# Kernel tuning notes

Measured on AMD Instinct MI355X. Metric: run time of the kernel, lower is better.

Reference implementation:

```python
import jax, jax.numpy as jnp
import numpy as np

N, E, F, H, C, G = 100000, 1600000, 128, 64, 40, 2048


def setup_inputs() -> dict:
    key = jax.random.key(0)
    ks = jax.random.split(key, 8)
    x = jax.random.normal(ks[0], (N, F), dtype=jnp.float32)
    edge_index = jax.random.randint(ks[1], (2, E), 0, N, dtype=jnp.int64)
    batch = jnp.sort(jax.random.randint(ks[2], (N,), 0, G, dtype=jnp.int64))
    def glorot(k, shp):
        fan_in, fan_out = shp
        s = jnp.sqrt(2.0 / (fan_in + fan_out))
        return jax.random.normal(k, shp, dtype=jnp.float32) * s
    return {
        "x": x, "edge_index": edge_index, "batch": batch,
        "pre_w": glorot(ks[3], (F, H)), "pre_b": jnp.zeros((H,), jnp.float32),
        "c1_w": glorot(ks[4], (H, H)), "c1_b": jnp.zeros((H,), jnp.float32),
        "n1_g": jnp.ones((H,), jnp.float32), "n1_b": jnp.zeros((H,), jnp.float32),
        "c2_w": glorot(ks[5], (H, H)), "c2_b": jnp.zeros((H,), jnp.float32),
        "n2_g": jnp.ones((H,), jnp.float32), "n2_b": jnp.zeros((H,), jnp.float32),
        "post_w": glorot(ks[6], (H, C)), "post_b": jnp.zeros((C,), jnp.float32),
    }


def _gcn_conv(h, src, dst, deg_isqrt, W, b):
    # GCNConv with self-loops and symmetric D^{-1/2}(A+I)D^{-1/2} normalization.
    hw = h @ W                                        # [N, H]
    coef = deg_isqrt[src] * deg_isqrt[dst]            # [E]
    msg = hw[src] * coef[:, None]                     # gather + scale
    agg = jax.ops.segment_sum(msg, dst, num_segments=N)
    agg = agg + hw * (deg_isqrt * deg_isqrt)[:, None]  # self-loop term
    return agg + b


def _layer_norm(h, g, b, eps=1e-5):
    mu = jnp.mean(h, axis=-1, keepdims=True)
    var = jnp.mean(jnp.square(h - mu), axis=-1, keepdims=True)
    return (h - mu) * jax.lax.rsqrt(var + eps) * g + b


def reference(x, edge_index, batch, pre_w, pre_b, c1_w, c1_b, n1_g, n1_b,
              c2_w, c2_b, n2_g, n2_b, post_w, post_b):
    src, dst = edge_index[0], edge_index[1]
    ones = jnp.ones((E,), dtype=x.dtype)
    deg = jax.ops.segment_sum(ones, dst, num_segments=N) + 1.0  # +1 self-loop
    deg_isqrt = jax.lax.rsqrt(deg)

    h = x @ pre_w + pre_b                              # pre-process MLP
    h1 = jax.nn.relu(_layer_norm(_gcn_conv(h, src, dst, deg_isqrt, c1_w, c1_b), n1_g, n1_b))
    h2 = jax.nn.relu(_layer_norm(_gcn_conv(h1, src, dst, deg_isqrt, c2_w, c2_b), n2_g, n2_b))
    skip = h1 + h2                                     # sum of skip connections
    readout = jax.ops.segment_sum(skip, batch, num_segments=G)  # sum pooling
    return readout @ post_w + post_b                   # [G, C]
```

## Files before the change

### kernel.cpp

```cpp
#include <hip/hip_runtime.h>
#include <hip/hip_fp16.h>

#define NN 100000
#define NE 1600000
#define FIN 128
#define HD 64
#define CO 40
#define NG 2048
#define NSB 196
#define SCAP 9216
#define GCAP 13312
#define CHUNK 4096
#define NSCAT ((NE + CHUNK - 1) / CHUNK)

__global__ __launch_bounds__(256) void setup_kernel(int* __restrict__ scur,
                                                    float* __restrict__ readout,
                                                    unsigned int* __restrict__ dummy) {
    int gid = blockIdx.x * 256 + threadIdx.x;
    if (gid < NG * HD) readout[gid] = 0.0f;
    if (gid < NSB) scur[gid * 16] = gid * SCAP;
    if (gid < HD / 2) dummy[gid] = 0u;
}

__global__ __launch_bounds__(1024) void scatter_super(const int* __restrict__ src,
                                                      const int* __restrict__ dst,
                                                      int* __restrict__ scur,
                                                      unsigned int* __restrict__ stmp) {
    __shared__ int hist[NSB];
    __shared__ int gbase[NSB];
    int tid = threadIdx.x;
    int e0 = blockIdx.x * CHUNK;
    int d[4], s[4];
    if (tid < NSB) hist[tid] = 0;
    __syncthreads();
#pragma unroll
    for (int r = 0; r < 4; r++) {
        int e = e0 + tid + r * 1024;
        d[r] = -1; s[r] = 0;
        if (e < NE) {
            d[r] = dst[e];
            s[r] = src[e];
            atomicAdd(&hist[d[r] >> 9], 1);
        }
    }
    __syncthreads();
    if (tid < NSB) {
        int c = hist[tid];
        gbase[tid] = (c > 0) ? atomicAdd(&scur[tid * 16], c) : 0;
        hist[tid] = 0;
    }
    __syncthreads();
#pragma unroll
    for (int r = 0; r < 4; r++) {
        if (d[r] >= 0) {
            int b = d[r] >> 9;
            int p = atomicAdd(&hist[b], 1);
            stmp[gbase[b] + p] = ((unsigned int)(d[r] & 511) << 17) | (unsigned int)s[r];
        }
    }
}

__global__ __launch_bounds__(1024) void group_sort(const int* __restrict__ scur,
                                                   const unsigned int* __restrict__ stmp,
                                                   unsigned int* __restrict__ ssrc,
                                                   int* __restrict__ offs,
                                                   int* __restrict__ degn,
                                                   float* __restrict__ di) {
    __shared__ int lh[512];
    __shared__ int sc[512];
    __shared__ int lcur[512];
    int g = blockIdx.x;
    int tid = threadIdx.x;
    int base = g * SCAP;
    int cnt = scur[g * 16] - base;
    if (tid < 512) lh[tid] = 0;
    __syncthreads();
    unsigned int uv[9];
#pragma unroll
    for (int r = 0; r < 9; r++) {
        int i = tid + r * 1024;
        uv[r] = 0xFFFFFFFFu;
        if (i < cnt) {
            uv[r] = stmp[base + i];
            atomicAdd(&lh[uv[r] >> 17], 1);
        }
    }
    __syncthreads();
    int h = 0, pd = 0;
    if (tid < 512) {
        h = lh[tid];
        pd = (h + 7) & ~7;
        sc[tid] = pd;
    }
    __syncthreads();
    for (int off = 1; off < 512; off <<= 1) {
        int v = 0;
        if (tid >= off && tid < 512) v = sc[tid - off];
        __syncthreads();
        if (tid < 512) sc[tid] += v;
        __syncthreads();
    }
    if (tid < 512) {
        int excl = sc[tid] - pd;
        lcur[tid] = excl;
        int node = g * 512 + tid;
        if (node < NN) {
            offs[node] = g * GCAP + excl;
            degn[node] = pd;
            di[node] = rsqrtf((float)h + 1.0f);
        }
        size_t gb = (size_t)g * GCAP;
        for (int q = h; q < pd; q++) ssrc[gb + excl + q] = (unsigned int)NN;
    }
    __syncthreads();
#pragma unroll
    for (int r = 0; r < 9; r++) {
        unsigned int u = uv[r];
        if (u != 0xFFFFFFFFu) {
            int dl = (int)(u >> 17);
            int pos = atomicAdd(&lcur[dl], 1);
            ssrc[(size_t)g * GCAP + pos] = u & 0x1FFFFu;
        }
    }
}

__global__ __launch_bounds__(256) void weff_kernel(const float* __restrict__ pre_w,
                                                   const float* __restrict__ pre_b,
                                                   const float* __restrict__ c1_w,
                                                   float* __restrict__ weff,
                                                   float* __restrict__ beff) {
    if (blockIdx.x < 32) {
        int o = blockIdx.x * 256 + threadIdx.x;
        int r = o >> 6, c = o & 63;
        float acc = 0.0f;
#pragma unroll 8
        for (int k = 0; k < HD; k++) acc = fmaf(pre_w[r * HD + k], c1_w[k * HD + c], acc);
        weff[o] = acc;
    } else {
        int c = threadIdx.x;
        if (c < HD) {
            float acc = 0.0f;
#pragma unroll 8
            for (int k = 0; k < HD; k++) acc = fmaf(pre_b[k], c1_w[k * HD + c], acc);
            beff[c] = acc;
        }
    }
}

__global__ __launch_bounds__(256) void gemm1_tiled(const float* __restrict__ x,
                                                   const float* __restrict__ w,
                                                   const float* __restrict__ b,
                                                   const float* __restrict__ di,
                                                   __half* __restrict__ hws) {
    __shared__ float wS[FIN * HD];
    __shared__ float xS[64 * 64];
    int tid = threadIdx.x;
    for (int i = tid; i < FIN * HD; i += 256) wS[i] = w[i];
    int tn = tid & 15, tf = tid >> 4;
    int f0 = tf * 4;
    float4 bv = ((const float4*)b)[tf];
    int ntiles = (NN + 63) >> 6;
    for (int t = blockIdx.x; t < ntiles; t += gridDim.x) {
        int nb = t << 6;
        float acc[4][4];
#pragma unroll
        for (int i = 0; i < 4; i++)
#pragma unroll
            for (int j = 0; j < 4; j++) acc[i][j] = 0.0f;
        for (int kh = 0; kh < 2; kh++) {
            __syncthreads();
            {
                int n_l = tid >> 4;
                int k4l = tid & 15;
                for (int r = 0; r < 4; r++) {
                    int n = n_l + r * 16;
                    int row = nb + n;
                    float4 v = make_float4(0.f, 0.f, 0.f, 0.f);
                    if (row < NN) v = ((const float4*)(x + (size_t)row * FIN))[kh * 16 + k4l];
                    int g = n >> 2, nl2 = n & 3;
                    const float* vp = (const float*)&v;
#pragma unroll
                    for (int j = 0; j < 4; j++) {
                        int k = k4l * 4 + j;
                        int gp = g ^ (k & 15);
                        xS[k * 64 + gp * 4 + nl2] = vp[j];
                    }
                }
            }
            __syncthreads();
#pragma unroll 4
            for (int kl = 0; kl < 64; kl++) {
                int gp = tn ^ (kl & 15);
                float4 xv = *(const float4*)&xS[kl * 64 + gp * 4];
                float4 wv = *(const float4*)&wS[(kh * 64 + kl) * 64 + f0];
                acc[0][0] = fmaf(xv.x, wv.x, acc[0][0]); acc[0][1] = fmaf(xv.x, wv.y, acc[0][1]);
                acc[0][2] = fmaf(xv.x, wv.z, acc[0][2]); acc[0][3] = fmaf(xv.x, wv.w, acc[0][3]);
                acc[1][0] = fmaf(xv.y, wv.x, acc[1][0]); acc[1][1] = fmaf(xv.y, wv.y, acc[1][1]);
                acc[1][2] = fmaf(xv.y, wv.z, acc[1][2]); acc[1][3] = fmaf(xv.y, wv.w, acc[1][3]);
                acc[2][0] = fmaf(xv.z, wv.x, acc[2][0]); acc[2][1] = fmaf(xv.z, wv.y, acc[2][1]);
                acc[2][2] = fmaf(xv.z, wv.z, acc[2][2]); acc[2][3] = fmaf(xv.z, wv.w, acc[2][3]);
                acc[3][0] = fmaf(xv.w, wv.x, acc[3][0]); acc[3][1] = fmaf(xv.w, wv.y, acc[3][1]);
                acc[3][2] = fmaf(xv.w, wv.z, acc[3][2]); acc[3][3] = fmaf(xv.w, wv.w, acc[3][3]);
            }
        }
        int n0 = nb + tn * 4;
#pragma unroll
        for (int i = 0; i < 4; i++) {
            int n = n0 + i;
            if (n < NN) {
                float dn = di[n];
                __half2 p0 = __floats2half2_rn((acc[i][0] + bv.x) * dn, (acc[i][1] + bv.y) * dn);
                __half2 p1 = __floats2half2_rn((acc[i][2] + bv.z) * dn, (acc[i][3] + bv.w) * dn);
                __half2* o = (__half2*)(hws + (size_t)n * HD + f0);
                o[0] = p0; o[1] = p1;
            }
        }
    }
}

__global__ __launch_bounds__(256) void conv_gemm_tiled(const __half* __restrict__ hin,
                                                       const float* __restrict__ w,
                                                       const float* __restrict__ di,
                                                       __half* __restrict__ hws) {
    __shared__ float wS[HD * HD];
    __shared__ float xS[64 * HD];
    int tid = threadIdx.x;
    for (int i = tid; i < HD * HD; i += 256) wS[i] = w[i];
    int tn = tid & 15, tf = tid >> 4;
    int f0 = tf * 4;
    int ntiles = (NN + 63) >> 6;
    for (int t = blockIdx.x; t < ntiles; t += gridDim.x) {
        int nb = t << 6;
        __syncthreads();
        {
            int n_l = tid >> 3;
            int k8 = tid & 7;
            union U { float4 f4; __half2 h2[4]; } u;
            for (int r = 0; r < 2; r++) {
                int n = n_l + r * 32;
                int row = nb + n;
                u.f4 = make_float4(0.f, 0.f, 0.f, 0.f);
                if (row < NN) u.f4 = ((const float4*)(hin + (size_t)row * HD))[k8];
                int g = n >> 2, nl2 = n & 3;
#pragma unroll
                for (int j = 0; j < 4; j++) {
                    float2 p = __half22float2(u.h2[j]);
                    int k = k8 * 8 + 2 * j;
                    int gp = g ^ (k & 15);
                    xS[k * 64 + gp * 4 + nl2] = p.x;
                    int k2 = k + 1;
                    int gp2 = g ^ (k2 & 15);
                    xS[k2 * 64 + gp2 * 4 + nl2] = p.y;
                }
            }
        }
        __syncthreads();
        float acc[4][4];
#pragma unroll
        for (int i = 0; i < 4; i++)
#pragma unroll
            for (int j = 0; j < 4; j++) acc[i][j] = 0.0f;
#pragma unroll 4
        for (int k = 0; k < HD; k++) {
            int gp = tn ^ (k & 15);
            float4 xv = *(const float4*)&xS[k * 64 + gp * 4];
            float4 wv = *(const float4*)&wS[k * 64 + f0];
            acc[0][0] = fmaf(xv.x, wv.x, acc[0][0]); acc[0][1] = fmaf(xv.x, wv.y, acc[0][1]);
            acc[0][2] = fmaf(xv.x, wv.z, acc[0][2]); acc[0][3] = fmaf(xv.x, wv.w, acc[0][3]);
            acc[1][0] = fmaf(xv.y, wv.x, acc[1][0]); acc[1][1] = fmaf(xv.y, wv.y, acc[1][1]);
            acc[1][2] = fmaf(xv.y, wv.z, acc[1][2]); acc[1][3] = fmaf(xv.y, wv.w, acc[1][3]);
            acc[2][0] = fmaf(xv.z, wv.x, acc[2][0]); acc[2][1] = fmaf(xv.z, wv.y, acc[2][1]);
            acc[2][2] = fmaf(xv.z, wv.z, acc[2][2]); acc[2][3] = fmaf(xv.z, wv.w, acc[2][3]);
            acc[3][0] = fmaf(xv.w, wv.x, acc[3][0]); acc[3][1] = fmaf(xv.w, wv.y, acc[3][1]);
            acc[3][2] = fmaf(xv.w, wv.z, acc[3][2]); acc[3][3] = fmaf(xv.w, wv.w, acc[3][3]);
        }
        int n0 = nb + tn * 4;
#pragma unroll
        for (int i = 0; i < 4; i++) {
            int n = n0 + i;
            if (n < NN) {
                float dn = di[n];
                __half2 p0 = __floats2half2_rn(acc[i][0] * dn, acc[i][1] * dn);
                __half2 p1 = __floats2half2_rn(acc[i][2] * dn, acc[i][3] * dn);
                __half2* o = (__half2*)(hws + (size_t)n * HD + f0);
                o[0] = p0; o[1] = p1;
            }
        }
    }
}

__device__ __forceinline__ void gather_node8(const int* __restrict__ offs,
                                             const int* __restrict__ pdeg,
                                             const unsigned int* __restrict__ ssrc,
                                             const __half* __restrict__ hws,
                                             int node, int fp, float acc[8]) {
    int i0 = offs[node];
    int deg = pdeg[node];
    const uint4* ip = (const uint4*)(ssrc + i0);
    union U { float4 f4; __half2 h2[4]; } u[8];
    __half2 hacc[4][4];
#pragma unroll
    for (int s = 0; s < 4; s++)
#pragma unroll
        for (int t = 0; t < 4; t++) hacc[s][t] = __floats2half2_rn(0.f, 0.f);
    u[0].f4 = ((const float4*)(hws + (size_t)node * HD))[fp];
#pragma unroll
    for (int t = 0; t < 4; t++) hacc[0][t] = u[0].h2[t];
    int nit = deg >> 3;
    if (nit > 0) {
        uint4 a0 = ip[0], b0 = ip[1];
        uint4 a1 = make_uint4(0u, 0u, 0u, 0u), b1 = a1;
        if (nit > 1) { a1 = ip[2]; b1 = ip[3]; }
        for (int it = 0; it < nit; ++it) {
            bool more = (it + 2 < nit);
            uint4 a2 = a1, b2 = b1;
            if (more) { a2 = ip[2 * it + 4]; b2 = ip[2 * it + 5]; }
            u[0].f4 = ((const float4*)(hws + (size_t)a0.x * HD))[fp];
            u[1].f4 = ((const float4*)(hws + (size_t)a0.y * HD))[fp];
            u[2].f4 = ((const float4*)(hws + (size_t)a0.z * HD))[fp];
            u[3].f4 = ((const float4*)(hws + (size_t)a0.w * HD))[fp];
            u[4].f4 = ((const float4*)(hws + (size_t)b0.x * HD))[fp];
            u[5].f4 = ((const float4*)(hws + (size_t)b0.y * HD))[fp];
            u[6].f4 = ((const float4*)(hws + (size_t)b0.z * HD))[fp];
            u[7].f4 = ((const float4*)(hws + (size_t)b0.w * HD))[fp];
#pragma unroll
            for (int q = 0; q < 8; q++)
#pragma unroll
                for (int t = 0; t < 4; t++)
                    hacc[q & 3][t] = __hadd2(hacc[q & 3][t], u[q].h2[t]);
            a0 = a1; b0 = b1;
            a1 = a2; b1 = b2;
        }
    }
#pragma unroll
    for (int t = 0; t < 4; t++) {
        float2 a = __half22float2(hacc[0][t]);
        float2 b = __half22float2(hacc[1][t]);
        float2 c = __half22float2(hacc[2][t]);
        float2 d = __half22float2(hacc[3][t]);
        acc[2 * t]     = (a.x + b.x) + (c.x + d.x);
        acc[2 * t + 1] = (a.y + b.y) + (c.y + d.y);
    }
}

__device__ __forceinline__ void ln8(float v[8], int fp,
                                    const float* __restrict__ g,
                                    const float* __restrict__ bb,
                                    float y[8]) {
    float su = 0.0f;
#pragma unroll
    for (int t = 0; t < 8; t++) su += v[t];
    su += __shfl_xor(su, 1, 64); su += __shfl_xor(su, 2, 64); su += __shfl_xor(su, 4, 64);
    float mu = su * (1.0f / HD);
    float q = 0.0f;
#pragma unroll
    for (int t = 0; t < 8; t++) { float d = v[t] - mu; q += d * d; }
    q += __shfl_xor(q, 1, 64); q += __shfl_xor(q, 2, 64); q += __shfl_xor(q, 4, 64);
    float rstd = rsqrtf(q * (1.0f / HD) + 1e-5f);
    float4 ga = ((const float4*)g)[fp * 2], gb = ((const float4*)g)[fp * 2 + 1];
    float4 ba = ((const float4*)bb)[fp * 2], bc = ((const float4*)bb)[fp * 2 + 1];
    float gv[8] = {ga.x, ga.y, ga.z, ga.w, gb.x, gb.y, gb.z, gb.w};
    float bv[8] = {ba.x, ba.y, ba.z, ba.w, bc.x, bc.y, bc.z, bc.w};
#pragma unroll
    for (int t = 0; t < 8; t++) y[t] = fmaxf((v[t] - mu) * rstd * gv[t] + bv[t], 0.0f);
}

__global__ __launch_bounds__(256, 4) void gather_ln(const int* __restrict__ offs,
                                                    const int* __restrict__ pdeg,
                                                    const unsigned int* __restrict__ ssrc,
                                                    const float* __restrict__ di,
                                                    const __half* __restrict__ hws,
                                                    const float* __restrict__ cb,
                                                    const float* __restrict__ g,
                                                    const float* __restrict__ bb,
                                                    __half* __restrict__ out) {
    int wv = threadIdx.x >> 6;
    int lane = threadIdx.x & 63;
    int fp = lane & 7, gg = lane >> 3;
    int node = blockIdx.x * 32 + wv * 8 + gg;
    float acc[8];
    gather_node8(offs, pdeg, ssrc, hws, node, fp, acc);
    float4 ca = ((const float4*)cb)[fp * 2], cc = ((const float4*)cb)[fp * 2 + 1];
    float cv[8] = {ca.x, ca.y, ca.z, ca.w, cc.x, cc.y, cc.z, cc.w};
    float dn = di[node];
    float v[8], y[8];
#pragma unroll
    for (int t = 0; t < 8; t++) v[t] = acc[t] * dn + cv[t];
    ln8(v, fp, g, bb, y);
    union U { float4 f4; __half2 h2[4]; } u;
#pragma unroll
    for (int t = 0; t < 4; t++) u.h2[t] = __floats2half2_rn(y[2 * t], y[2 * t + 1]);
    ((float4*)(out + (size_t)node * HD))[fp] = u.f4;
}

__global__ __launch_bounds__(256, 4) void gather_ln_pool(const int* __restrict__ offs,
                                                         const int* __restrict__ pdeg,
                                                         const unsigned int* __restrict__ ssrc,
                                                         const float* __restrict__ di,
                                                         const __half* __restrict__ hws,
                                                         const float* __restrict__ cb,
                                                         const float* __restrict__ g,
                                                         const float* __restrict__ bb,
                                                         const __half* __restrict__ h1,
                                                         const int* __restrict__ batch,
                                                         float* __restrict__ readout) {
    __shared__ float ls[32][65];
    __shared__ int lb[32];
    int wv = threadIdx.x >> 6;
    int lane = threadIdx.x & 63;
    int fp = lane & 7, gg = lane >> 3;
    int node = blockIdx.x * 32 + wv * 8 + gg;
    float acc[8];
    gather_node8(offs, pdeg, ssrc, hws, node, fp, acc);
    float4 ca = ((const float4*)cb)[fp * 2], cc = ((const float4*)cb)[fp * 2 + 1];
    float cv[8] = {ca.x, ca.y, ca.z, ca.w, cc.x, cc.y, cc.z, cc.w};
    float dn = di[node];
    float v[8], y[8];
#pragma unroll
    for (int t = 0; t < 8; t++) v[t] = acc[t] * dn + cv[t];
    ln8(v, fp, g, bb, y);
    union U { float4 f4; __half2 h2[4]; } u;
    u.f4 = ((const float4*)(h1 + (size_t)node * HD))[fp];
    int row = wv * 8 + gg;
#pragma unroll
    for (int t = 0; t < 4; t++) {
        float2 p = __half22float2(u.h2[t]);
        ls[row][fp * 8 + 2 * t]     = y[2 * t] + p.x;
        ls[row][fp * 8 + 2 * t + 1] = y[2 * t + 1] + p.y;
    }
    if (fp == 0) lb[row] = batch[node];
    int r0 = wv * 8;
    int bu = lb[r0];
    bool uni = true;
#pragma unroll
    for (int r = 1; r < 8; r++) uni = uni && (lb[r0 + r] == bu);
    int f = lane;
    if (uni) {
        float s2 = 0.0f;
#pragma unroll
        for (int r = 0; r < 8; r++) s2 += ls[r0 + r][f];
        atomicAdd(&readout[(size_t)bu * HD + f], s2);
    } else {
        float s2 = ls[r0][f];
        int bprev = lb[r0];
#pragma unroll
        for (int r = 1; r < 8; r++) {
            int bn = lb[r0 + r];
            if (bn == bprev) {
                s2 += ls[r0 + r][f];
            } else {
                atomicAdd(&readout[(size_t)bprev * HD + f], s2);
                s2 = ls[r0 + r][f];
                bprev = bn;
            }
        }
        atomicAdd(&readout[(size_t)bprev * HD + f], s2);
    }
}

__global__ __launch_bounds__(256) void out_gemm(const float* __restrict__ r,
                                                const float* __restrict__ w,
                                                const float* __restrict__ b,
                                                float* __restrict__ out) {
    __shared__ float lw[HD * CO];
    for (int i = threadIdx.x; i < HD * CO; i += 256) lw[i] = w[i];
    __syncthreads();
    int grp = blockIdx.x * 4 + (threadIdx.x >> 6);
    int c = threadIdx.x & 63;
    if (grp >= NG || c >= CO) return;
    const float* rr = r + (size_t)grp * HD;
    float acc = b[c];
#pragma unroll 8
    for (int k = 0; k < HD; k++) acc = fmaf(rr[k], lw[k * CO + c], acc);
    out[(size_t)grp * CO + c] = acc;
}

extern "C" void kernel_launch(void* const* d_in, const int* in_sizes, int n_in,
                              void* d_out, int out_size, void* d_ws, size_t ws_size,
                              hipStream_t stream) {
    const float* x      = (const float*)d_in[0];
    const int*   ei     = (const int*)d_in[1];
    const int*   batch  = (const int*)d_in[2];
    const float* pre_w  = (const float*)d_in[3];
    const float* pre_b  = (const float*)d_in[4];
    const float* c1_w   = (const float*)d_in[5];
    const float* c1_b   = (const float*)d_in[6];
    const float* n1_g   = (const float*)d_in[7];
    const float* n1_b   = (const float*)d_in[8];
    const float* c2_w   = (const float*)d_in[9];
    const float* c2_b   = (const float*)d_in[10];
    const float* n2_g   = (const float*)d_in[11];
    const float* n2_b   = (const float*)d_in[12];
    const float* post_w = (const float*)d_in[13];
    const float* post_b = (const float*)d_in[14];

    const int* src = ei;
    const int* dst = ei + NE;

    char* p = (char*)d_ws;
    int*          scur    = (int*)p;          p += (size_t)NSB * 16 * 4;
    int*          offs    = (int*)p;          p += (size_t)NN * 4;
    int*          degn    = (int*)p;          p += (size_t)NN * 4;
    float*        di      = (float*)p;        p += (size_t)NN * 4;
    float*        weff    = (float*)p;        p += (size_t)FIN * HD * 4;
    float*        beff    = (float*)p;        p += 256;
    unsigned int* stmp    = (unsigned int*)p; p += (size_t)NSB * SCAP * 4;
    unsigned int* ssrc    = (unsigned int*)p; p += (size_t)NSB * GCAP * 4;
    float*        readout = (float*)p;        p += (size_t)NG * HD * 4;
    __half*       hws     = (__half*)p;       p += (size_t)(NN + 8) * HD * 2;
    __half*       h1      = (__half*)p;       p += (size_t)NN * HD * 2;

    setup_kernel<<<(NG * HD + 255) / 256, 256, 0, stream>>>(scur, readout,
                                                            (unsigned int*)(hws + (size_t)NN * HD));

    scatter_super<<<NSCAT, 1024, 0, stream>>>(src, dst, scur, stmp);
    group_sort<<<NSB, 1024, 0, stream>>>(scur, stmp, ssrc, offs, degn, di);

    weff_kernel<<<33, 256, 0, stream>>>(pre_w, pre_b, c1_w, weff, beff);

    gemm1_tiled<<<768, 256, 0, stream>>>(x, weff, beff, di, hws);
    gather_ln<<<NN / 32, 256, 0, stream>>>(offs, degn, ssrc, di, hws, c1_b, n1_g, n1_b, h1);

    conv_gemm_tiled<<<1280, 256, 0, stream>>>(h1, c2_w, di, hws);
    gather_ln_pool<<<NN / 32, 256, 0, stream>>>(offs, degn, ssrc, di, hws, c2_b, n2_g, n2_b, h1, batch, readout);

    out_gemm<<<(NG + 3) / 4, 256, 0, stream>>>(readout, post_w, post_b, (float*)d_out);
}
```

Baseline: 275.7 us.

## Replace FP32 tiled GEMMs with fp16 MFMA matrix-core kernels

The two dense node GEMMs (the fused pre-MLP times conv1 weight, and the conv2 weight GEMM) now use the 16x16x32 fp16 MFMA instruction instead of scalar FMA tiles. The weight-preparation kernel now also writes transposed fp16 copies of both weight matrices, so the MFMA B fragments load straight from padded LDS. Input x is converted to fp16 in registers, which lowers the precision of the first GEMM's inputs. The output is stored as scalar half writes, one per element, rather than packed pairs.

```diff
diff --git a/kernel.cpp b/kernel.cpp
--- a/kernel.cpp
+++ b/kernel.cpp
@@ -12,6 +12,9 @@
 #define GCAP 13312
 #define CHUNK 4096
 #define NSCAT ((NE + CHUNK - 1) / CHUNK)
+
+typedef _Float16 half8 __attribute__((ext_vector_type(8)));
+typedef float floatx4 __attribute__((ext_vector_type(4)));
 
 __global__ __launch_bounds__(256) void setup_kernel(int* __restrict__ scur,
                                                     float* __restrict__ readout,
@@ -127,16 +130,19 @@
 __global__ __launch_bounds__(256) void weff_kernel(const float* __restrict__ pre_w,
                                                    const float* __restrict__ pre_b,
                                                    const float* __restrict__ c1_w,
-                                                   float* __restrict__ weff,
-                                                   float* __restrict__ beff) {
-    if (blockIdx.x < 32) {
-        int o = blockIdx.x * 256 + threadIdx.x;
+                                                   const float* __restrict__ c2_w,
+                                                   _Float16* __restrict__ wth,
+                                                   float* __restrict__ beff,
+                                                   _Float16* __restrict__ wt2h) {
+    int b = blockIdx.x;
+    if (b < 32) {
+        int o = b * 256 + threadIdx.x;
         int r = o >> 6, c = o & 63;
         float acc = 0.0f;
 #pragma unroll 8
         for (int k = 0; k < HD; k++) acc = fmaf(pre_w[r * HD + k], c1_w[k * HD + c], acc);
-        weff[o] = acc;
-    } else {
+        wth[c * FIN + r] = (_Float16)acc;
+    } else if (b == 32) {
         int c = threadIdx.x;
         if (c < HD) {
             float acc = 0.0f;
@@ -144,147 +150,101 @@
             for (int k = 0; k < HD; k++) acc = fmaf(pre_b[k], c1_w[k * HD + c], acc);
             beff[c] = acc;
         }
-    }
-}
-
-__global__ __launch_bounds__(256) void gemm1_tiled(const float* __restrict__ x,
-                                                   const float* __restrict__ w,
-                                                   const float* __restrict__ b,
-                                                   const float* __restrict__ di,
-                                                   __half* __restrict__ hws) {
-    __shared__ float wS[FIN * HD];
-    __shared__ float xS[64 * 64];
+    } else {
+        int o = (b - 33) * 256 + threadIdx.x;
+        int r = o >> 6, c = o & 63;
+        wt2h[c * HD + r] = (_Float16)c2_w[o];
+    }
+}
+
+__global__ __launch_bounds__(256, 4) void gemm1_mfma(const float* __restrict__ x,
+                                                     const _Float16* __restrict__ wt,
+                                                     const float* __restrict__ beff,
+                                                     const float* __restrict__ di,
+                                                     __half* __restrict__ hws) {
+    __shared__ _Float16 wS[64 * 136];
     int tid = threadIdx.x;
-    for (int i = tid; i < FIN * HD; i += 256) wS[i] = w[i];
-    int tn = tid & 15, tf = tid >> 4;
-    int f0 = tf * 4;
-    float4 bv = ((const float4*)b)[tf];
-    int ntiles = (NN + 63) >> 6;
-    for (int t = blockIdx.x; t < ntiles; t += gridDim.x) {
-        int nb = t << 6;
-        float acc[4][4];
-#pragma unroll
-        for (int i = 0; i < 4; i++)
-#pragma unroll
-            for (int j = 0; j < 4; j++) acc[i][j] = 0.0f;
-        for (int kh = 0; kh < 2; kh++) {
-            __syncthreads();
-            {
-                int n_l = tid >> 4;
-                int k4l = tid & 15;
-                for (int r = 0; r < 4; r++) {
-                    int n = n_l + r * 16;
-                    int row = nb + n;
-                    float4 v = make_float4(0.f, 0.f, 0.f, 0.f);
-                    if (row < NN) v = ((const float4*)(x + (size_t)row * FIN))[kh * 16 + k4l];
-                    int g = n >> 2, nl2 = n & 3;
-                    const float* vp = (const float*)&v;
-#pragma unroll
-                    for (int j = 0; j < 4; j++) {
-                        int k = k4l * 4 + j;
-                        int gp = g ^ (k & 15);
-                        xS[k * 64 + gp * 4 + nl2] = vp[j];
-                    }
-                }
-            }
-            __syncthreads();
-#pragma unroll 4
-            for (int kl = 0; kl < 64; kl++) {
-                int gp = tn ^ (kl & 15);
-                float4 xv = *(const float4*)&xS[kl * 64 + gp * 4];
-                float4 wv = *(const float4*)&wS[(kh * 64 + kl) * 64 + f0];
-                acc[0][0] = fmaf(xv.x, wv.x, acc[0][0]); acc[0][1] = fmaf(xv.x, wv.y, acc[0][1]);
-                acc[0][2] = fmaf(xv.x, wv.z, acc[0][2]); acc[0][3] = fmaf(xv.x, wv.w, acc[0][3]);
-                acc[1][0] = fmaf(xv.y, wv.x, acc[1][0]); acc[1][1] = fmaf(xv.y, wv.y, acc[1][1]);
-                acc[1][2] = fmaf(xv.y, wv.z, acc[1][2]); acc[1][3] = fmaf(xv.y, wv.w, acc[1][3]);
-                acc[2][0] = fmaf(xv.z, wv.x, acc[2][0]); acc[2][1] = fmaf(xv.z, wv.y, acc[2][1]);
-                acc[2][2] = fmaf(xv.z, wv.z, acc[2][2]); acc[2][3] = fmaf(xv.z, wv.w, acc[2][3]);
-                acc[3][0] = fmaf(xv.w, wv.x, acc[3][0]); acc[3][1] = fmaf(xv.w, wv.y, acc[3][1]);
-                acc[3][2] = fmaf(xv.w, wv.z, acc[3][2]); acc[3][3] = fmaf(xv.w, wv.w, acc[3][3]);
-            }
-        }
-        int n0 = nb + tn * 4;
-#pragma unroll
-        for (int i = 0; i < 4; i++) {
-            int n = n0 + i;
-            if (n < NN) {
-                float dn = di[n];
-                __half2 p0 = __floats2half2_rn((acc[i][0] + bv.x) * dn, (acc[i][1] + bv.y) * dn);
-                __half2 p1 = __floats2half2_rn((acc[i][2] + bv.z) * dn, (acc[i][3] + bv.w) * dn);
-                __half2* o = (__half2*)(hws + (size_t)n * HD + f0);
-                o[0] = p0; o[1] = p1;
-            }
-        }
-    }
-}
-
-__global__ __launch_bounds__(256) void conv_gemm_tiled(const __half* __restrict__ hin,
-                                                       const float* __restrict__ w,
-                                                       const float* __restrict__ di,
-                                                       __half* __restrict__ hws) {
-    __shared__ float wS[HD * HD];
-    __shared__ float xS[64 * HD];
+    for (int i = tid; i < 1024; i += 256) {
+        int n = i >> 4, k0 = (i & 15) * 8;
+        *(uint4*)&wS[n * 136 + k0] = ((const uint4*)wt)[i];
+    }
+    __syncthreads();
+    int wv = tid >> 6, lane = tid & 63;
+    int l15 = lane & 15, lg = lane >> 4;
+    int rbase = blockIdx.x * 64 + wv * 16;
+    if (rbase >= NN) return;
+    half8 bf[4][4];
+#pragma unroll
+    for (int ks = 0; ks < 4; ks++)
+#pragma unroll
+        for (int ns = 0; ns < 4; ns++)
+            bf[ks][ns] = *(const half8*)&wS[(ns * 16 + l15) * 136 + ks * 32 + lg * 8];
+    floatx4 acc[4];
+#pragma unroll
+    for (int ns = 0; ns < 4; ns++) acc[ns] = (floatx4){0.f, 0.f, 0.f, 0.f};
+    const float* xrow = x + (size_t)(rbase + l15) * FIN;
+#pragma unroll
+    for (int ks = 0; ks < 4; ks++) {
+        float4 lo = *(const float4*)(xrow + ks * 32 + lg * 8);
+        float4 hi = *(const float4*)(xrow + ks * 32 + lg * 8 + 4);
+        half8 a;
+        a[0] = (_Float16)lo.x; a[1] = (_Float16)lo.y; a[2] = (_Float16)lo.z; a[3] = (_Float16)lo.w;
+        a[4] = (_Float16)hi.x; a[5] = (_Float16)hi.y; a[6] = (_Float16)hi.z; a[7] = (_Float16)hi.w;
+#pragma unroll
+        for (int ns = 0; ns < 4; ns++)
+            acc[ns] = __builtin_amdgcn_mfma_f32_16x16x32_f16(a, bf[ks][ns], acc[ns], 0, 0, 0);
+    }
+    int r0 = rbase + lg * 4;
+#pragma unroll
+    for (int ns = 0; ns < 4; ns++) {
+        float be = beff[ns * 16 + l15];
+#pragma unroll
+        for (int r = 0; r < 4; r++) {
+            float dn = di[r0 + r];
+            hws[(size_t)(r0 + r) * HD + ns * 16 + l15] = __float2half((acc[ns][r] + be) * dn);
+        }
+    }
+}
+
+__global__ __launch_bounds__(256, 4) void conv_gemm_mfma(const __half* __restrict__ hin,
+                                                         const _Float16* __restrict__ wt2,
+                                                         const float* __restrict__ di,
+                                                         __half* __restrict__ hws) {
+    __shared__ _Float16 wS[64 * 72];
     int tid = threadIdx.x;
-    for (int i = tid; i < HD * HD; i += 256) wS[i] = w[i];
-    int tn = tid & 15, tf = tid >> 4;
-    int f0 = tf * 4;
-    int ntiles = (NN + 63) >> 6;
-    for (int t = blockIdx.x; t < ntiles; t += gridDim.x) {
-        int nb = t << 6;
-        __syncthreads();
-        {
-            int n_l = tid >> 3;
-            int k8 = tid & 7;
-            union U { float4 f4; __half2 h2[4]; } u;
-            for (int r = 0; r < 2; r++) {
-                int n = n_l + r * 32;
-                int row = nb + n;
-                u.f4 = make_float4(0.f, 0.f, 0.f, 0.f);
-                if (row < NN) u.f4 = ((const float4*)(hin + (size_t)row * HD))[k8];
-                int g = n >> 2, nl2 = n & 3;
-#pragma unroll
-                for (int j = 0; j < 4; j++) {
-                    float2 p = __half22float2(u.h2[j]);
-                    int k = k8 * 8 + 2 * j;
-                    int gp = g ^ (k & 15);
-                    xS[k * 64 + gp * 4 + nl2] = p.x;
-                    int k2 = k + 1;
-                    int gp2 = g ^ (k2 & 15);
-                    xS[k2 * 64 + gp2 * 4 + nl2] = p.y;
-                }
-            }
-        }
-        __syncthreads();
-        float acc[4][4];
-#pragma unroll
-        for (int i = 0; i < 4; i++)
-#pragma unroll
-            for (int j = 0; j < 4; j++) acc[i][j] = 0.0f;
-#pragma unroll 4
-        for (int k = 0; k < HD; k++) {
-            int gp = tn ^ (k & 15);
-            float4 xv = *(const float4*)&xS[k * 64 + gp * 4];
-            float4 wv = *(const float4*)&wS[k * 64 + f0];
-            acc[0][0] = fmaf(xv.x, wv.x, acc[0][0]); acc[0][1] = fmaf(xv.x, wv.y, acc[0][1]);
-            acc[0][2] = fmaf(xv.x, wv.z, acc[0][2]); acc[0][3] = fmaf(xv.x, wv.w, acc[0][3]);
-            acc[1][0] = fmaf(xv.y, wv.x, acc[1][0]); acc[1][1] = fmaf(xv.y, wv.y, acc[1][1]);
-            acc[1][2] = fmaf(xv.y, wv.z, acc[1][2]); acc[1][3] = fmaf(xv.y, wv.w, acc[1][3]);
-            acc[2][0] = fmaf(xv.z, wv.x, acc[2][0]); acc[2][1] = fmaf(xv.z, wv.y, acc[2][1]);
-            acc[2][2] = fmaf(xv.z, wv.z, acc[2][2]); acc[2][3] = fmaf(xv.z, wv.w, acc[2][3]);
-            acc[3][0] = fmaf(xv.w, wv.x, acc[3][0]); acc[3][1] = fmaf(xv.w, wv.y, acc[3][1]);
-            acc[3][2] = fmaf(xv.w, wv.z, acc[3][2]); acc[3][3] = fmaf(xv.w, wv.w, acc[3][3]);
-        }
-        int n0 = nb + tn * 4;
-#pragma unroll
-        for (int i = 0; i < 4; i++) {
-            int n = n0 + i;
-            if (n < NN) {
-                float dn = di[n];
-                __half2 p0 = __floats2half2_rn(acc[i][0] * dn, acc[i][1] * dn);
-                __half2 p1 = __floats2half2_rn(acc[i][2] * dn, acc[i][3] * dn);
-                __half2* o = (__half2*)(hws + (size_t)n * HD + f0);
-                o[0] = p0; o[1] = p1;
-            }
+    for (int i = tid; i < 512; i += 256) {
+        int n = i >> 3, k0 = (i & 7) * 8;
+        *(uint4*)&wS[n * 72 + k0] = ((const uint4*)wt2)[i];
+    }
+    __syncthreads();
+    int wv = tid >> 6, lane = tid & 63;
+    int l15 = lane & 15, lg = lane >> 4;
+    int rbase = blockIdx.x * 64 + wv * 16;
+    if (rbase >= NN) return;
+    half8 bf[2][4];
+#pragma unroll
+    for (int ks = 0; ks < 2; ks++)
+#pragma unroll
+        for (int ns = 0; ns < 4; ns++)
+            bf[ks][ns] = *(const half8*)&wS[(ns * 16 + l15) * 72 + ks * 32 + lg * 8];
+    floatx4 acc[4];
+#pragma unroll
+    for (int ns = 0; ns < 4; ns++) acc[ns] = (floatx4){0.f, 0.f, 0.f, 0.f};
+    const __half* hrow = hin + (size_t)(rbase + l15) * HD;
+#pragma unroll
+    for (int ks = 0; ks < 2; ks++) {
+        half8 a = *(const half8*)(hrow + ks * 32 + lg * 8);
+#pragma unroll
+        for (int ns = 0; ns < 4; ns++)
+            acc[ns] = __builtin_amdgcn_mfma_f32_16x16x32_f16(a, bf[ks][ns], acc[ns], 0, 0, 0);
+    }
+    int r0 = rbase + lg * 4;
+#pragma unroll
+    for (int ns = 0; ns < 4; ns++) {
+#pragma unroll
+        for (int r = 0; r < 4; r++) {
+            float dn = di[r0 + r];
+            hws[(size_t)(r0 + r) * HD + ns * 16 + l15] = __float2half(acc[ns][r] * dn);
         }
     }
 }
@@ -502,7 +462,8 @@
     int*          offs    = (int*)p;          p += (size_t)NN * 4;
     int*          degn    = (int*)p;          p += (size_t)NN * 4;
     float*        di      = (float*)p;        p += (size_t)NN * 4;
-    float*        weff    = (float*)p;        p += (size_t)FIN * HD * 4;
+    _Float16*     wth     = (_Float16*)p;     p += (size_t)FIN * HD * 2;
+    _Float16*     wt2h    = (_Float16*)p;     p += (size_t)HD * HD * 2;
     float*        beff    = (float*)p;        p += 256;
     unsigned int* stmp    = (unsigned int*)p; p += (size_t)NSB * SCAP * 4;
     unsigned int* ssrc    = (unsigned int*)p; p += (size_t)NSB * GCAP * 4;
@@ -516,12 +477,12 @@
     scatter_super<<<NSCAT, 1024, 0, stream>>>(src, dst, scur, stmp);
     group_sort<<<NSB, 1024, 0, stream>>>(scur, stmp, ssrc, offs, degn, di);
 
-    weff_kernel<<<33, 256, 0, stream>>>(pre_w, pre_b, c1_w, weff, beff);
-
-    gemm1_tiled<<<768, 256, 0, stream>>>(x, weff, beff, di, hws);
+    weff_kernel<<<49, 256, 0, stream>>>(pre_w, pre_b, c1_w, c2_w, wth, beff, wt2h);
+
+    gemm1_mfma<<<(NN + 63) / 64, 256, 0, stream>>>(x, wth, beff, di, hws);
     gather_ln<<<NN / 32, 256, 0, stream>>>(offs, degn, ssrc, di, hws, c1_b, n1_g, n1_b, h1);
 
-    conv_gemm_tiled<<<1280, 256, 0, stream>>>(h1, c2_w, di, hws);
+    conv_gemm_mfma<<<(NN + 63) / 64, 256, 0, stream>>>(h1, wt2h, di, hws);
     gather_ln_pool<<<NN / 32, 256, 0, stream>>>(offs, degn, ssrc, di, hws, c2_b, n2_g, n2_b, h1, batch, readout);
 
     out_gemm<<<(NG + 3) / 4, 256, 0, stream>>>(readout, post_w, post_b, (float*)d_out);
```

Result: faster. 243.5 us (-11.7%).
